# Kernel tuning notes

Hardware: AMD Instinct MI355X
Metric: run time of the kernel (lower is better)

## Reference

```python
import jax, jax.numpy as jnp
import numpy as np

B, S, D = 2, 2048, 1024
H = 16
DH = D // H


def _layernorm(x, g, b, eps=1e-5):
    mu = jnp.mean(x, axis=-1, keepdims=True)
    var = jnp.var(x, axis=-1, keepdims=True)
    return (x - mu) * jax.lax.rsqrt(var + eps) * g + b


def setup_inputs() -> dict:
    key = jax.random.key(0)
    ks = jax.random.split(key, 8)
    s = lambda fan_in: 1.0 / np.sqrt(fan_in)
    return {
        "x": jax.random.normal(ks[0], (B, S, D), dtype=jnp.float32),
        "ln1_g": jnp.ones((D,), jnp.float32),
        "ln1_b": jnp.zeros((D,), jnp.float32),
        "w_qkv": jax.random.uniform(ks[1], (D, 3 * D), jnp.float32, -s(D), s(D)),
        "b_qkv": jnp.zeros((3 * D,), jnp.float32),
        "w_out": jax.random.uniform(ks[2], (D, D), jnp.float32, -s(D), s(D)),
        "b_out": jnp.zeros((D,), jnp.float32),
        "ln2_g": jnp.ones((D,), jnp.float32),
        "ln2_b": jnp.zeros((D,), jnp.float32),
        "w1": jax.random.uniform(ks[3], (D, 4 * D), jnp.float32, -s(D), s(D)),
        "b1": jnp.zeros((4 * D,), jnp.float32),
        "w2": jax.random.uniform(ks[4], (4 * D, D), jnp.float32, -s(4 * D), s(4 * D)),
        "b2": jnp.zeros((D,), jnp.float32),
    }


def reference(x, ln1_g, ln1_b, w_qkv, b_qkv, w_out, b_out,
              ln2_g, ln2_b, w1, b1, w2, b2):
    scale = DH ** -0.5
    residual = x
    h = _layernorm(x, ln1_g, ln1_b)
    qkv = h @ w_qkv + b_qkv                      # [B,S,3D]
    q, k, v = jnp.split(qkv, 3, axis=-1)
    # [B,S,D] -> [B,H,S,DH]
    split_heads = lambda t: t.reshape(B, S, H, DH).transpose(0, 2, 1, 3)
    q, k, v = map(split_heads, (q, k, v))
    scores = jnp.einsum("bhsd,bhtd->bhst", q, k) * scale  # full O(S^2) matrix
    attn = jax.nn.softmax(scores, axis=-1)
    out = jnp.einsum("bhst,bhtd->bhsd", attn, v)
    out = out.transpose(0, 2, 1, 3).reshape(B, S, D)
    out = out @ w_out + b_out                    # dropout is identity at eval
    x = residual + out
    residual = x
    h = _layernorm(x, ln2_g, ln2_b)
    h = jax.nn.gelu(h @ w1 + b1, approximate=False)
    h = h @ w2 + b2
    return residual + h
```

## Files before the change

### kernel.cpp

```cpp
#include <hip/hip_runtime.h>
#include <hip/hip_bf16.h>
#include <math.h>

#define Bc 2
#define Sc 2048
#define Dc 1024
#define Hc 16
#define DHc 64
#define Mc (Bc*Sc)

typedef __attribute__((ext_vector_type(8))) short bf16x8;
typedef __attribute__((ext_vector_type(4))) float f32x4;

#define QSCALE 0.18033688f

__device__ __forceinline__ ushort f2bf(float f){
  union { float f; uint32_t u; } c; c.f = f;
  uint32_t u = c.u;
  return (ushort)((u + 0x7fffu + ((u >> 16) & 1u)) >> 16);
}
__device__ __forceinline__ float fast_exp2(float x){
#if __has_builtin(__builtin_amdgcn_exp2f)
  return __builtin_amdgcn_exp2f(x);
#else
  return exp2f(x);
#endif
}
__device__ __forceinline__ uint32_t cvt_pk_bf16(float a, float b){
  uint32_t r;
  asm("v_cvt_pk_bf16_f32 %0, %1, %2" : "=v"(r) : "v"(a), "v"(b));
  return r;
}

__device__ __forceinline__ void stage16(const void* g, void* lbase, int lane){
#if __has_builtin(__builtin_amdgcn_global_load_lds)
  __builtin_amdgcn_global_load_lds(
      (const __attribute__((address_space(1))) void*)g,
      (__attribute__((address_space(3))) void*)lbase, 16, 0, 0);
#else
  *(int4*)((char*)lbase + lane*16) = *(const int4*)g;
#endif
}

__global__ __launch_bounds__(256) void tcast(const float* __restrict__ w,
                                             ushort* __restrict__ wt,
                                             int K, int N){
  __shared__ float t[32][33];
  int kb = blockIdx.y * 32, nb = blockIdx.x * 32;
  int tx = threadIdx.x & 31, ty = threadIdx.x >> 5;
  #pragma unroll
  for (int i = 0; i < 4; i++)
    t[ty + 8*i][tx] = w[(size_t)(kb + ty + 8*i) * N + nb + tx];
  __syncthreads();
  #pragma unroll
  for (int i = 0; i < 4; i++)
    wt[(size_t)(nb + ty + 8*i) * K + kb + tx] = f2bf(t[tx][ty + 8*i]);
}

__global__ __launch_bounds__(256) void ln_bf16(const float* __restrict__ x,
                                               const float* __restrict__ g,
                                               const float* __restrict__ b,
                                               ushort* __restrict__ out){
  int row = blockIdx.x;
  const float4 xv = reinterpret_cast<const float4*>(x + (size_t)row * Dc)[threadIdx.x];
  float s  = xv.x + xv.y + xv.z + xv.w;
  float sq = xv.x*xv.x + xv.y*xv.y + xv.z*xv.z + xv.w*xv.w;
  #pragma unroll
  for (int m = 1; m < 64; m <<= 1){ s += __shfl_xor(s, m); sq += __shfl_xor(sq, m); }
  __shared__ float ss[4], ssq[4];
  int wv = threadIdx.x >> 6;
  if ((threadIdx.x & 63) == 0){ ss[wv] = s; ssq[wv] = sq; }
  __syncthreads();
  s  = ss[0] + ss[1] + ss[2] + ss[3];
  sq = ssq[0] + ssq[1] + ssq[2] + ssq[3];
  float mu  = s * (1.0f / Dc);
  float var = sq * (1.0f / Dc) - mu * mu;
  float rstd = rsqrtf(var + 1e-5f);
  float4 gv = reinterpret_cast<const float4*>(g)[threadIdx.x];
  float4 bv = reinterpret_cast<const float4*>(b)[threadIdx.x];
  ushort o[4];
  o[0] = f2bf((xv.x - mu) * rstd * gv.x + bv.x);
  o[1] = f2bf((xv.y - mu) * rstd * gv.y + bv.y);
  o[2] = f2bf((xv.z - mu) * rstd * gv.z + bv.z);
  o[3] = f2bf((xv.w - mu) * rstd * gv.w + bv.w);
  *reinterpret_cast<uint2*>(out + (size_t)row * Dc + threadIdx.x * 4) =
      *reinterpret_cast<uint2*>(o);
}

template<int EPI>
__global__ __launch_bounds__(256) void gemm128(
    const ushort* __restrict__ A, const ushort* __restrict__ BT,
    const float* __restrict__ bias,
    ushort* __restrict__ outb,
    ushort* __restrict__ oq, ushort* __restrict__ ok, ushort* __restrict__ ov,
    int N, int K){
  __shared__ short As[2][128*32];
  __shared__ short Bs[2][128*32];

  const int fid = blockIdx.x;
  const int q8 = gridDim.x >> 3;
  const int id2 = (fid & 7) * q8 + (fid >> 3);
  const int nbx = N / 128;
  const int nb = id2 % nbx, mb = id2 / nbx;

  const int tid = threadIdx.x;
  const int wave = tid >> 6, lane = tid & 63;
  const int wm = wave >> 1, wn = wave & 1;
  const int lr = lane & 15, lg = lane >> 4;

  f32x4 acc[4][4] = {};

  const int sr = tid >> 2;
  const int sc = ((tid & 3) * 8) ^ ((sr & 3) * 8);
  const ushort* Ag = A  + (size_t)(mb * 128 + sr) * K + sc;
  const ushort* Bg = BT + (size_t)(nb * 128 + sr) * K + sc;
  const int nK = K >> 5;

  {
    char* Ab = (char*)&As[0][0] + wave * 1024;
    char* Bb = (char*)&Bs[0][0] + wave * 1024;
    stage16(Ag,                 Ab,        lane);
    stage16(Ag + (size_t)64*K,  Ab + 4096, lane);
    stage16(Bg,                 Bb,        lane);
    stage16(Bg + (size_t)64*K,  Bb + 4096, lane);
  }
  __syncthreads();

  const int rsz = (lr & 3) * 8;

  for (int kt = 0; kt < nK; ++kt){
    const int cur = kt & 1;
    if (kt + 1 < nK){
      const int ko = (kt + 1) * 32;
      char* Ab = (char*)&As[cur ^ 1][0] + wave * 1024;
      char* Bb = (char*)&Bs[cur ^ 1][0] + wave * 1024;
      stage16(Ag + ko,                 Ab,        lane);
      stage16(Ag + (size_t)64*K + ko,  Ab + 4096, lane);
      stage16(Bg + ko,                 Bb,        lane);
      stage16(Bg + (size_t)64*K + ko,  Bb + 4096, lane);
    }
    bf16x8 af[4], bfr[4];
    #pragma unroll
    for (int mt = 0; mt < 4; mt++)
      af[mt] = *reinterpret_cast<const bf16x8*>(
          &As[cur][(wm*64 + mt*16 + lr)*32 + ((lg*8) ^ rsz)]);
    #pragma unroll
    for (int nt = 0; nt < 4; nt++)
      bfr[nt] = *reinterpret_cast<const bf16x8*>(
          &Bs[cur][(wn*64 + nt*16 + lr)*32 + ((lg*8) ^ rsz)]);
    #pragma unroll
    for (int mt = 0; mt < 4; mt++)
      #pragma unroll
      for (int nt = 0; nt < 4; nt++)
        acc[mt][nt] = __builtin_amdgcn_mfma_f32_16x16x32_bf16(af[mt], bfr[nt], acc[mt][nt], 0, 0, 0);
    __syncthreads();
  }

  if (EPI == 0){
    #pragma unroll
    for (int mt = 0; mt < 4; mt++){
      const int gm0 = mb * 128 + wm * 64 + mt * 16 + lg * 4;
      const int bb = gm0 >> 11, s0 = gm0 & 2047;
      #pragma unroll
      for (int nt = 0; nt < 4; nt++){
        const int gn = nb * 128 + wn * 64 + nt * 16 + lr;
        const float bv = bias[gn];
        const int p = gn >> 10, d = gn & 1023;
        const int hh = d >> 6, dh = d & 63;
        const int bh = bb * Hc + hh;
        if (p == 2){
          ushort pk[4];
          #pragma unroll
          for (int r = 0; r < 4; r++) pk[r] = f2bf(acc[mt][nt][r] + bv);
          *reinterpret_cast<uint2*>(ov + ((size_t)bh * DHc + dh) * Sc + s0) =
              *reinterpret_cast<uint2*>(pk);
        } else if (p == 0){
          #pragma unroll
          for (int r = 0; r < 4; r++)
            oq[((size_t)bh * Sc + s0 + r) * DHc + dh] = f2bf((acc[mt][nt][r] + bv) * QSCALE);
        } else {
          #pragma unroll
          for (int r = 0; r < 4; r++)
            ok[((size_t)bh * Sc + s0 + r) * DHc + dh] = f2bf(acc[mt][nt][r] + bv);
        }
      }
    }
  } else {
    #pragma unroll
    for (int mt = 0; mt < 4; mt++){
      #pragma unroll
      for (int nt = 0; nt < 4; nt++){
        #pragma unroll
        for (int r = 0; r < 4; r++){
          const int gm = mb * 128 + wm * 64 + mt * 16 + lg * 4 + r;
          const int gn = nb * 128 + wn * 64 + nt * 16 + lr;
          float val = acc[mt][nt][r] + bias[gn];
          float ge = 0.5f * val * (1.0f + erff(val * 0.70710678118f));
          outb[(size_t)gm * N + gn] = f2bf(ge);
        }
      }
    }
  }
}

__global__ __launch_bounds__(256) void gemm_res64(
    const ushort* __restrict__ A, const ushort* __restrict__ BT,
    const float* __restrict__ bias, const float* __restrict__ res,
    float* __restrict__ outf, int N, int K){
  __shared__ short As[2][128*32];
  __shared__ short Bs[2][64*32];

  const int fid = blockIdx.x;
  const int q8 = gridDim.x >> 3;
  const int id2 = (fid & 7) * q8 + (fid >> 3);
  const int nbx = N / 64;
  const int nb = id2 % nbx, mb = id2 / nbx;

  const int tid = threadIdx.x;
  const int wave = tid >> 6, lane = tid & 63;
  const int wm = wave >> 1, wn = wave & 1;
  const int lr = lane & 15, lg = lane >> 4;

  f32x4 acc[4][2] = {};

  const int sr = tid >> 2;
  const int sc = ((tid & 3) * 8) ^ ((sr & 3) * 8);
  const ushort* Ag = A  + (size_t)(mb * 128 + sr) * K + sc;
  const ushort* Bg = BT + (size_t)(nb * 64  + sr) * K + sc;
  const int nK = K >> 5;

  {
    char* Ab = (char*)&As[0][0] + wave * 1024;
    char* Bb = (char*)&Bs[0][0] + wave * 1024;
    stage16(Ag,                Ab,        lane);
    stage16(Ag + (size_t)64*K, Ab + 4096, lane);
    stage16(Bg,                Bb,        lane);
  }
  __syncthreads();

  const int rsz = (lr & 3) * 8;

  for (int kt = 0; kt < nK; ++kt){
    const int cur = kt & 1;
    if (kt + 1 < nK){
      const int ko = (kt + 1) * 32;
      char* Ab = (char*)&As[cur ^ 1][0] + wave * 1024;
      char* Bb = (char*)&Bs[cur ^ 1][0] + wave * 1024;
      stage16(Ag + ko,                Ab,        lane);
      stage16(Ag + (size_t)64*K + ko, Ab + 4096, lane);
      stage16(Bg + ko,                Bb,        lane);
    }
    bf16x8 af[4], bfr[2];
    #pragma unroll
    for (int mt = 0; mt < 4; mt++)
      af[mt] = *reinterpret_cast<const bf16x8*>(
          &As[cur][(wm*64 + mt*16 + lr)*32 + ((lg*8) ^ rsz)]);
    #pragma unroll
    for (int nt = 0; nt < 2; nt++)
      bfr[nt] = *reinterpret_cast<const bf16x8*>(
          &Bs[cur][(wn*32 + nt*16 + lr)*32 + ((lg*8) ^ rsz)]);
    #pragma unroll
    for (int mt = 0; mt < 4; mt++)
      #pragma unroll
      for (int nt = 0; nt < 2; nt++)
        acc[mt][nt] = __builtin_amdgcn_mfma_f32_16x16x32_bf16(af[mt], bfr[nt], acc[mt][nt], 0, 0, 0);
    __syncthreads();
  }

  #pragma unroll
  for (int mt = 0; mt < 4; mt++){
    #pragma unroll
    for (int nt = 0; nt < 2; nt++){
      #pragma unroll
      for (int r = 0; r < 4; r++){
        const int gm = mb * 128 + wm * 64 + mt * 16 + lg * 4 + r;
        const int gn = nb * 64 + wn * 32 + nt * 16 + lr;
        const size_t i = (size_t)gm * N + gn;
        outf[i] = acc[mt][nt][r] + bias[gn] + res[i];
      }
    }
  }
}

__global__ __launch_bounds__(256) void flash_attn(const ushort* __restrict__ q,
                                                  const ushort* __restrict__ k,
                                                  const ushort* __restrict__ vt,
                                                  ushort* __restrict__ ctx){
  const int bh = blockIdx.y;
  const int q0 = blockIdx.x * 64;
  const int b  = bh >> 4, h = bh & 15;
  const int tid = threadIdx.x, wave = tid >> 6, lane = tid & 63;
  const int lr = lane & 15, lg = lane >> 4;

  __shared__ short Kt[2][64*64];
  __shared__ short Vt[64*64];
  __shared__ short Ps[4][16][68];

  const int g8  = lane & 7;
  const int kr0 = wave * 8 + (lane >> 3);
  const int kcol = (g8 ^ (kr0 & 7)) * 8;
  const ushort* kg0 = k + (size_t)bh * Sc * DHc + (size_t)kr0 * DHc + kcol;
  const ushort* kg1 = kg0 + 32 * DHc;
  char* Kl = (char*)&Kt[0][0] + wave * 1024;
  const int KBUFB = 64 * 64 * 2;

  const int vrow = tid >> 3, vg8 = tid & 7;
  const int vcol = (vg8 ^ (vrow & 7)) * 8;
  const ushort* vg0 = vt + (size_t)bh * DHc * Sc + (size_t)vrow * Sc + vcol;
  const ushort* vg1 = vg0 + (size_t)32 * Sc;

  bf16x8 qf0, qf1;
  {
    const ushort* qp = q + (size_t)bh * Sc * DHc + (size_t)(q0 + wave * 16 + lr) * DHc + lg * 8;
    qf0 = *reinterpret_cast<const bf16x8*>(qp);
    qf1 = *reinterpret_cast<const bf16x8*>(qp + 32);
  }

  f32x4 o[4] = {};
  float lps = 0.f;
  constexpr int NTILES = Sc / 64;

  stage16(kg0, Kl,        lane);
  stage16(kg1, Kl + 4096, lane);
  {
    int4 w0 = *reinterpret_cast<const int4*>(vg0);
    int4 w1 = *reinterpret_cast<const int4*>(vg1);
    *reinterpret_cast<int4*>((char*)&Vt[0] + tid * 16)        = w0;
    *reinterpret_cast<int4*>((char*)&Vt[0] + 4096 + tid * 16) = w1;
  }
  __syncthreads();

  const int swz = (lr & 7) * 8;

  for (int kt = 0; kt < NTILES; ++kt){
    const int cur = kt & 1;
    int4 vr0, vr1;
    if (kt + 1 < NTILES){
      const int nx = (cur ^ 1) * KBUFB;
      stage16(kg0 + (size_t)(kt + 1) * 64 * DHc, Kl + nx,        lane);
      stage16(kg1 + (size_t)(kt + 1) * 64 * DHc, Kl + nx + 4096, lane);
      vr0 = *reinterpret_cast<const int4*>(vg0 + (kt + 1) * 64);
      vr1 = *reinterpret_cast<const int4*>(vg1 + (kt + 1) * 64);
    }

    f32x4 sacc[4];
    __builtin_amdgcn_s_setprio(1);
    #pragma unroll
    for (int nt = 0; nt < 4; nt++){
      const int rb = (nt * 16 + lr) * 64;
      bf16x8 b0 = *reinterpret_cast<const bf16x8*>(&Kt[cur][rb + ((lg * 8) ^ swz)]);
      bf16x8 b1 = *reinterpret_cast<const bf16x8*>(&Kt[cur][rb + ((32 + lg * 8) ^ swz)]);
      f32x4 z = {0.f, 0.f, 0.f, 0.f};
      z = __builtin_amdgcn_mfma_f32_16x16x32_bf16(b0, qf0, z, 0, 0, 0);
      z = __builtin_amdgcn_mfma_f32_16x16x32_bf16(b1, qf1, z, 0, 0, 0);
      sacc[nt] = z;
    }
    __builtin_amdgcn_s_setprio(0);

    #pragma unroll
    for (int nt = 0; nt < 4; nt++){
      float p0 = fast_exp2(sacc[nt][0]);
      float p1 = fast_exp2(sacc[nt][1]);
      float p2 = fast_exp2(sacc[nt][2]);
      float p3 = fast_exp2(sacc[nt][3]);
      lps += (p0 + p1) + (p2 + p3);
      uint2 wd;
      wd.x = cvt_pk_bf16(p0, p1);
      wd.y = cvt_pk_bf16(p2, p3);
      *reinterpret_cast<uint2*>(&Ps[wave][lr][nt * 16 + lg * 4]) = wd;
    }

    bf16x8 pf0 = *reinterpret_cast<const bf16x8*>(&Ps[wave][lr][lg * 8]);
    bf16x8 pf1 = *reinterpret_cast<const bf16x8*>(&Ps[wave][lr][32 + lg * 8]);
    __builtin_amdgcn_s_setprio(1);
    #pragma unroll
    for (int nt = 0; nt < 4; nt++){
      const int rb = (nt * 16 + lr) * 64;
      bf16x8 v0 = *reinterpret_cast<const bf16x8*>(&Vt[rb + ((lg * 8) ^ swz)]);
      bf16x8 v1 = *reinterpret_cast<const bf16x8*>(&Vt[rb + ((32 + lg * 8) ^ swz)]);
      o[nt] = __builtin_amdgcn_mfma_f32_16x16x32_bf16(pf0, v0, o[nt], 0, 0, 0);
      o[nt] = __builtin_amdgcn_mfma_f32_16x16x32_bf16(pf1, v1, o[nt], 0, 0, 0);
    }
    __builtin_amdgcn_s_setprio(0);

    __syncthreads();
    if (kt + 1 < NTILES){
      *reinterpret_cast<int4*>((char*)&Vt[0] + tid * 16)        = vr0;
      *reinterpret_cast<int4*>((char*)&Vt[0] + 4096 + tid * 16) = vr1;
      __syncthreads();
    }
  }

  lps += __shfl_xor(lps, 16);
  lps += __shfl_xor(lps, 32);

  #pragma unroll
  for (int j = 0; j < 4; j++){
    float inv = 1.0f / __shfl(lps, lg * 4 + j);
    int s = q0 + wave * 16 + lg * 4 + j;
    ushort* op = ctx + ((size_t)b * Sc + s) * Dc + h * DHc;
    #pragma unroll
    for (int nt = 0; nt < 4; nt++)
      op[nt * 16 + lr] = f2bf(o[nt][j] * inv);
  }
}

extern "C" void kernel_launch(void* const* d_in, const int* in_sizes, int n_in,
                              void* d_out, int out_size, void* d_ws, size_t ws_size,
                              hipStream_t stream){
  const float* x     = (const float*)d_in[0];
  const float* ln1_g = (const float*)d_in[1];
  const float* ln1_b = (const float*)d_in[2];
  const float* w_qkv = (const float*)d_in[3];
  const float* b_qkv = (const float*)d_in[4];
  const float* w_out = (const float*)d_in[5];
  const float* b_out = (const float*)d_in[6];
  const float* ln2_g = (const float*)d_in[7];
  const float* ln2_b = (const float*)d_in[8];
  const float* w1    = (const float*)d_in[9];
  const float* b1    = (const float*)d_in[10];
  const float* w2    = (const float*)d_in[11];
  const float* b2    = (const float*)d_in[12];
  float* out = (float*)d_out;

  char* ws = (char*)d_ws;
  size_t off = 0;
  ushort* wqkvT = (ushort*)(ws + off); off += (size_t)3072 * 1024 * 2;
  ushort* woutT = (ushort*)(ws + off); off += (size_t)1024 * 1024 * 2;
  ushort* w1T   = (ushort*)(ws + off); off += (size_t)4096 * 1024 * 2;
  ushort* w2T   = (ushort*)(ws + off); off += (size_t)1024 * 4096 * 2;
  ushort* hln   = (ushort*)(ws + off); off += (size_t)Mc * Dc * 2;
  ushort* qbuf  = (ushort*)(ws + off); off += (size_t)32 * Sc * DHc * 2;
  ushort* kbuf  = (ushort*)(ws + off); off += (size_t)32 * Sc * DHc * 2;
  ushort* vtbuf = (ushort*)(ws + off); off += (size_t)32 * Sc * DHc * 2;
  ushort* ctx   = (ushort*)(ws + off); off += (size_t)Mc * Dc * 2;
  float*  x1    = (float*)(ws + off);  off += (size_t)Mc * Dc * 4;
  ushort* act   = qbuf;

  tcast<<<dim3(3072 / 32, 1024 / 32), 256, 0, stream>>>(w_qkv, wqkvT, 1024, 3072);
  tcast<<<dim3(1024 / 32, 1024 / 32), 256, 0, stream>>>(w_out, woutT, 1024, 1024);
  tcast<<<dim3(4096 / 32, 1024 / 32), 256, 0, stream>>>(w1,    w1T,   1024, 4096);
  tcast<<<dim3(1024 / 32, 4096 / 32), 256, 0, stream>>>(w2,    w2T,   4096, 1024);

  ln_bf16<<<Mc, 256, 0, stream>>>(x, ln1_g, ln1_b, hln);

  gemm128<0><<<(3072/128) * (Mc/128), 256, 0, stream>>>(
      hln, wqkvT, b_qkv, nullptr, qbuf, kbuf, vtbuf, 3072, 1024);

  flash_attn<<<dim3(Sc / 64, 32), 256, 0, stream>>>(qbuf, kbuf, vtbuf, ctx);

  gemm_res64<<<(1024/64) * (Mc/128), 256, 0, stream>>>(
      ctx, woutT, b_out, x, x1, 1024, 1024);

  ln_bf16<<<Mc, 256, 0, stream>>>(x1, ln2_g, ln2_b, hln);

  gemm128<2><<<(4096/128) * (Mc/128), 256, 0, stream>>>(
      hln, w1T, b1, act, nullptr, nullptr, nullptr, 4096, 1024);

  gemm_res64<<<(1024/64) * (Mc/128), 256, 0, stream>>>(
      act, w2T, b2, x1, out, 1024, 4096);
}
```

Before: 274.5 us.

## Double GEMM K-tile to 64 with 8-way swizzle and replace erf GELU with sigmoid approximation

Both GEMM kernels now stage a 64-wide K slice per iteration instead of 32, using a new 8-row by 8-chunk XOR swizzle for the LDS layout. Each iteration then runs two MFMA sub-steps. This halves the number of barriers and loop iterations and should give more work per synchronisation, at the cost of twice the LDS use per block, which may lower occupancy. Separately, the exact erf GELU in the FFN epilogue is replaced by a tanh-style sigmoid approximation built from exp2 and rcp, which changes numerics slightly.

```diff
diff --git a/kernel.cpp b/kernel.cpp
--- a/kernel.cpp
+++ b/kernel.cpp
@@ -25,6 +25,19 @@
 #else
   return exp2f(x);
 #endif
+}
+__device__ __forceinline__ float fast_rcp(float x){
+#if __has_builtin(__builtin_amdgcn_rcpf)
+  return __builtin_amdgcn_rcpf(x);
+#else
+  return 1.0f / x;
+#endif
+}
+__device__ __forceinline__ float fast_gelu(float x){
+  float x2 = x * x;
+  float y  = x * (2.30220826f + 0.10294442f * x2);
+  float t  = fast_exp2(fminf(y, 80.f));
+  return x * t * fast_rcp(t + 1.0f);
 }
 __device__ __forceinline__ uint32_t cvt_pk_bf16(float a, float b){
   uint32_t r;
@@ -94,8 +107,8 @@
     ushort* __restrict__ outb,
     ushort* __restrict__ oq, ushort* __restrict__ ok, ushort* __restrict__ ov,
     int N, int K){
-  __shared__ short As[2][128*32];
-  __shared__ short Bs[2][128*32];
+  __shared__ short As[2][128*64];
+  __shared__ short Bs[2][128*64];
 
   const int fid = blockIdx.x;
   const int q8 = gridDim.x >> 3;
@@ -110,49 +123,53 @@
 
   f32x4 acc[4][4] = {};
 
-  const int sr = tid >> 2;
-  const int sc = ((tid & 3) * 8) ^ ((sr & 3) * 8);
-  const ushort* Ag = A  + (size_t)(mb * 128 + sr) * K + sc;
-  const ushort* Bg = BT + (size_t)(nb * 128 + sr) * K + sc;
-  const int nK = K >> 5;
+  const int srow = wave * 8 + (lane >> 3);
+  const int sgc  = ((lane & 7) ^ (lane >> 3)) * 8;
+  const ushort* Ag = A  + (size_t)(mb * 128 + srow) * K + sgc;
+  const ushort* Bg = BT + (size_t)(nb * 128 + srow) * K + sgc;
+  const int nK = K >> 6;
 
   {
     char* Ab = (char*)&As[0][0] + wave * 1024;
     char* Bb = (char*)&Bs[0][0] + wave * 1024;
-    stage16(Ag,                 Ab,        lane);
-    stage16(Ag + (size_t)64*K,  Ab + 4096, lane);
-    stage16(Bg,                 Bb,        lane);
-    stage16(Bg + (size_t)64*K,  Bb + 4096, lane);
+    #pragma unroll
+    for (int c = 0; c < 4; c++){
+      stage16(Ag + (size_t)c * 32 * K, Ab + c * 4096, lane);
+      stage16(Bg + (size_t)c * 32 * K, Bb + c * 4096, lane);
+    }
   }
   __syncthreads();
 
-  const int rsz = (lr & 3) * 8;
+  const int swzr = (lr & 7) * 8;
 
   for (int kt = 0; kt < nK; ++kt){
     const int cur = kt & 1;
     if (kt + 1 < nK){
-      const int ko = (kt + 1) * 32;
+      const int ko = (kt + 1) * 64;
       char* Ab = (char*)&As[cur ^ 1][0] + wave * 1024;
       char* Bb = (char*)&Bs[cur ^ 1][0] + wave * 1024;
-      stage16(Ag + ko,                 Ab,        lane);
-      stage16(Ag + (size_t)64*K + ko,  Ab + 4096, lane);
-      stage16(Bg + ko,                 Bb,        lane);
-      stage16(Bg + (size_t)64*K + ko,  Bb + 4096, lane);
-    }
-    bf16x8 af[4], bfr[4];
-    #pragma unroll
-    for (int mt = 0; mt < 4; mt++)
-      af[mt] = *reinterpret_cast<const bf16x8*>(
-          &As[cur][(wm*64 + mt*16 + lr)*32 + ((lg*8) ^ rsz)]);
-    #pragma unroll
-    for (int nt = 0; nt < 4; nt++)
-      bfr[nt] = *reinterpret_cast<const bf16x8*>(
-          &Bs[cur][(wn*64 + nt*16 + lr)*32 + ((lg*8) ^ rsz)]);
-    #pragma unroll
-    for (int mt = 0; mt < 4; mt++)
+      #pragma unroll
+      for (int c = 0; c < 4; c++){
+        stage16(Ag + (size_t)c * 32 * K + ko, Ab + c * 4096, lane);
+        stage16(Bg + (size_t)c * 32 * K + ko, Bb + c * 4096, lane);
+      }
+    }
+    #pragma unroll
+    for (int ks = 0; ks < 2; ks++){
+      const int col = (ks * 32 + lg * 8) ^ swzr;
+      bf16x8 af[4], bfr[4];
+      #pragma unroll
+      for (int mt = 0; mt < 4; mt++)
+        af[mt] = *reinterpret_cast<const bf16x8*>(&As[cur][(wm*64 + mt*16 + lr)*64 + col]);
       #pragma unroll
       for (int nt = 0; nt < 4; nt++)
-        acc[mt][nt] = __builtin_amdgcn_mfma_f32_16x16x32_bf16(af[mt], bfr[nt], acc[mt][nt], 0, 0, 0);
+        bfr[nt] = *reinterpret_cast<const bf16x8*>(&Bs[cur][(wn*64 + nt*16 + lr)*64 + col]);
+      #pragma unroll
+      for (int mt = 0; mt < 4; mt++)
+        #pragma unroll
+        for (int nt = 0; nt < 4; nt++)
+          acc[mt][nt] = __builtin_amdgcn_mfma_f32_16x16x32_bf16(af[mt], bfr[nt], acc[mt][nt], 0, 0, 0);
+    }
     __syncthreads();
   }
 
@@ -194,9 +211,7 @@
         for (int r = 0; r < 4; r++){
           const int gm = mb * 128 + wm * 64 + mt * 16 + lg * 4 + r;
           const int gn = nb * 128 + wn * 64 + nt * 16 + lr;
-          float val = acc[mt][nt][r] + bias[gn];
-          float ge = 0.5f * val * (1.0f + erff(val * 0.70710678118f));
-          outb[(size_t)gm * N + gn] = f2bf(ge);
+          outb[(size_t)gm * N + gn] = f2bf(fast_gelu(acc[mt][nt][r] + bias[gn]));
         }
       }
     }
@@ -207,8 +222,8 @@
     const ushort* __restrict__ A, const ushort* __restrict__ BT,
     const float* __restrict__ bias, const float* __restrict__ res,
     float* __restrict__ outf, int N, int K){
-  __shared__ short As[2][128*32];
-  __shared__ short Bs[2][64*32];
+  __shared__ short As[2][128*64];
+  __shared__ short Bs[2][64*64];
 
   const int fid = blockIdx.x;
   const int q8 = gridDim.x >> 3;
@@ -223,47 +238,55 @@
 
   f32x4 acc[4][2] = {};
 
-  const int sr = tid >> 2;
-  const int sc = ((tid & 3) * 8) ^ ((sr & 3) * 8);
-  const ushort* Ag = A  + (size_t)(mb * 128 + sr) * K + sc;
-  const ushort* Bg = BT + (size_t)(nb * 64  + sr) * K + sc;
-  const int nK = K >> 5;
+  const int srow = wave * 8 + (lane >> 3);
+  const int sgc  = ((lane & 7) ^ (lane >> 3)) * 8;
+  const ushort* Ag = A  + (size_t)(mb * 128 + srow) * K + sgc;
+  const ushort* Bg = BT + (size_t)(nb * 64  + srow) * K + sgc;
+  const int nK = K >> 6;
 
   {
     char* Ab = (char*)&As[0][0] + wave * 1024;
     char* Bb = (char*)&Bs[0][0] + wave * 1024;
-    stage16(Ag,                Ab,        lane);
-    stage16(Ag + (size_t)64*K, Ab + 4096, lane);
-    stage16(Bg,                Bb,        lane);
+    #pragma unroll
+    for (int c = 0; c < 4; c++)
+      stage16(Ag + (size_t)c * 32 * K, Ab + c * 4096, lane);
+    #pragma unroll
+    for (int c = 0; c < 2; c++)
+      stage16(Bg + (size_t)c * 32 * K, Bb + c * 4096, lane);
   }
   __syncthreads();
 
-  const int rsz = (lr & 3) * 8;
+  const int swzr = (lr & 7) * 8;
 
   for (int kt = 0; kt < nK; ++kt){
     const int cur = kt & 1;
     if (kt + 1 < nK){
-      const int ko = (kt + 1) * 32;
+      const int ko = (kt + 1) * 64;
       char* Ab = (char*)&As[cur ^ 1][0] + wave * 1024;
       char* Bb = (char*)&Bs[cur ^ 1][0] + wave * 1024;
-      stage16(Ag + ko,                Ab,        lane);
-      stage16(Ag + (size_t)64*K + ko, Ab + 4096, lane);
-      stage16(Bg + ko,                Bb,        lane);
-    }
-    bf16x8 af[4], bfr[2];
-    #pragma unroll
-    for (int mt = 0; mt < 4; mt++)
-      af[mt] = *reinterpret_cast<const bf16x8*>(
-          &As[cur][(wm*64 + mt*16 + lr)*32 + ((lg*8) ^ rsz)]);
-    #pragma unroll
-    for (int nt = 0; nt < 2; nt++)
-      bfr[nt] = *reinterpret_cast<const bf16x8*>(
-          &Bs[cur][(wn*32 + nt*16 + lr)*32 + ((lg*8) ^ rsz)]);
-    #pragma unroll
-    for (int mt = 0; mt < 4; mt++)
+      #pragma unroll
+      for (int c = 0; c < 4; c++)
+        stage16(Ag + (size_t)c * 32 * K + ko, Ab + c * 4096, lane);
+      #pragma unroll
+      for (int c = 0; c < 2; c++)
+        stage16(Bg + (size_t)c * 32 * K + ko, Bb + c * 4096, lane);
+    }
+    #pragma unroll
+    for (int ks = 0; ks < 2; ks++){
+      const int col = (ks * 32 + lg * 8) ^ swzr;
+      bf16x8 af[4], bfr[2];
+      #pragma unroll
+      for (int mt = 0; mt < 4; mt++)
+        af[mt] = *reinterpret_cast<const bf16x8*>(&As[cur][(wm*64 + mt*16 + lr)*64 + col]);
       #pragma unroll
       for (int nt = 0; nt < 2; nt++)
-        acc[mt][nt] = __builtin_amdgcn_mfma_f32_16x16x32_bf16(af[mt], bfr[nt], acc[mt][nt], 0, 0, 0);
+        bfr[nt] = *reinterpret_cast<const bf16x8*>(&Bs[cur][(wn*32 + nt*16 + lr)*64 + col]);
+      #pragma unroll
+      for (int mt = 0; mt < 4; mt++)
+        #pragma unroll
+        for (int nt = 0; nt < 2; nt++)
+          acc[mt][nt] = __builtin_amdgcn_mfma_f32_16x16x32_bf16(af[mt], bfr[nt], acc[mt][nt], 0, 0, 0);
+    }
     __syncthreads();
   }
 
```

Measured after the change: 250.4 us. -8.8%, faster.
